# Performance work log

Hardware: AMD Instinct MI355X
Metric: run time of the kernel (lower is better)

The kernel has to match this reference:

```python
import jax, jax.numpy as jnp
import numpy as np

NUM_EXPERTS = 8
TOP_K = 2
B, S, D = 8, 8192, 256


def setup_inputs() -> dict:
    key = jax.random.key(0)
    ks = jax.random.split(key, 4)
    scale = 1.0 / np.sqrt(D).astype(np.float32)
    return {
        "input_embeddings": jax.random.normal(ks[0], (B, S, D), jnp.float32),
        "router_w": jax.random.normal(ks[1], (NUM_EXPERTS, D), jnp.float32) * scale,
        "w1": jax.random.normal(ks[2], (NUM_EXPERTS, D, D), jnp.float32) * scale,
        "b1": jnp.zeros((NUM_EXPERTS, D), jnp.float32),
        "w2": jax.random.normal(ks[3], (NUM_EXPERTS, D, D), jnp.float32) * scale,
        "b2": jnp.zeros((NUM_EXPERTS, D), jnp.float32),
    }


def _moe(tokens, router_w, w1, b1, w2, b2):
    # tokens: [N, D]
    N = tokens.shape[0]
    E = router_w.shape[0]
    # Router in float32 (matches torch .float() cast)
    logits = tokens.astype(jnp.float32) @ router_w.astype(jnp.float32).T  # [N, E]
    probs = jax.nn.softmax(logits, axis=-1)
    rw, re = jax.lax.top_k(probs, TOP_K)  # [N, K]
    if TOP_K > 1:
        rw = rw / jnp.maximum(rw.sum(-1, keepdims=True), 1e-12)
    rw = rw.astype(tokens.dtype)
    # Dense combine weights: zero for unselected experts -> identical math to
    # the torch gather/index_add dispatch (weight 0 == not routed).
    combine = jnp.zeros((N, E), tokens.dtype).at[jnp.arange(N)[:, None], re].set(rw)
    out = tokens  # residual: tokens + weighted expert outputs
    for e in range(E):  # small fixed expert loop
        h = jax.nn.gelu(tokens @ w1[e] + b1[e], approximate=False)
        y = h @ w2[e] + b2[e]
        out = out + combine[:, e:e + 1] * y
    return out


def reference(input_embeddings, router_w, w1, b1, w2, b2):
    b, s, d = input_embeddings.shape
    tokens = input_embeddings.reshape(b * s, d)
    return _moe(tokens, router_w, w1, b1, w2, b2).reshape(b, s, d)
```

## Files before the change

### kernel.cpp

```cpp
#include <hip/hip_runtime.h>
#include <hip/hip_bf16.h>

#define NEXP 8
#define DD 256

typedef __attribute__((ext_vector_type(8))) short  bf16x8;
typedef __attribute__((ext_vector_type(4))) float  f32x4;

__device__ __forceinline__ unsigned short f2bf(float f) {
    union { float f; unsigned int u; } v; v.f = f;
    unsigned int r = (v.u + 0x7FFFu + ((v.u >> 16) & 1u)) >> 16;
    return (unsigned short)r;
}

__device__ __forceinline__ float gelu_exact(float x) {
    return 0.5f * x * (1.0f + erff(x * 0.70710678118654752f));
}

__global__ __launch_bounds__(256)
void prep_weights(const float* __restrict__ w1, const float* __restrict__ w2,
                  unsigned short* __restrict__ w1t, unsigned short* __restrict__ w2t)
{
    __shared__ float tile[64][65];
    const int m  = blockIdx.x >> 7;
    const int e  = (blockIdx.x >> 4) & 7;
    const int ko = (blockIdx.x >> 2) & 3;
    const int no = blockIdx.x & 3;
    const float* src = m ? w2 : w1;
    unsigned short* dst = m ? w2t : w1t;
    const size_t base = ((size_t)e << 16);

    #pragma unroll
    for (int i = 0; i < 16; ++i) {
        int r = i * 4 + (threadIdx.x >> 6);
        int c = threadIdx.x & 63;
        tile[r][c] = src[base + (size_t)(ko * 64 + r) * DD + no * 64 + c];
    }
    __syncthreads();
    #pragma unroll
    for (int i = 0; i < 8; ++i) {
        int n  = i * 8 + (threadIdx.x >> 5);
        int k2 = (threadIdx.x & 31) * 2;
        unsigned int val = (unsigned int)f2bf(tile[k2][n])
                         | ((unsigned int)f2bf(tile[k2 + 1][n]) << 16);
        *(unsigned int*)(dst + base + (size_t)(no * 64 + n) * DD + ko * 64 + k2) = val;
    }
}

__global__ __launch_bounds__(256)
void router_kernel(const float* __restrict__ X, const float* __restrict__ RW,
                   unsigned int* __restrict__ re, float* __restrict__ rwgt,
                   int* __restrict__ bcnt, int N)
{
    __shared__ float rws[NEXP * DD];
    __shared__ int hist[16];
    const int tid = threadIdx.x;
    if (tid < 16) hist[tid] = 0;
    for (int i = tid; i < NEXP * DD / 4; i += 256)
        ((float4*)rws)[i] = ((const float4*)RW)[i];
    __syncthreads();
    const int wave = tid >> 6, lane = tid & 63;

    for (int it = 0; it < 16; ++it) {
        int t = blockIdx.x * 64 + wave * 16 + it;
        float4 xv = *(const float4*)(X + (size_t)t * DD + lane * 4);
        float lg[NEXP];
        #pragma unroll
        for (int e = 0; e < NEXP; ++e) {
            float4 wv = *(const float4*)(rws + e * DD + lane * 4);
            lg[e] = xv.x * wv.x + xv.y * wv.y + xv.z * wv.z + xv.w * wv.w;
        }
        #pragma unroll
        for (int e = 0; e < NEXP; ++e) {
            #pragma unroll
            for (int off = 32; off; off >>= 1)
                lg[e] += __shfl_xor(lg[e], off);
        }
        int e0 = 0; float l0 = lg[0];
        #pragma unroll
        for (int e = 1; e < NEXP; ++e) if (lg[e] > l0) { l0 = lg[e]; e0 = e; }
        int e1 = -1; float l1 = -3.4e38f;
        #pragma unroll
        for (int e = 0; e < NEXP; ++e) if (e != e0 && lg[e] > l1) { l1 = lg[e]; e1 = e; }
        float d   = expf(l1 - l0);
        float w0  = 1.0f / (1.0f + d);
        float w1v = d / (1.0f + d);
        if (lane == 0) {
            re[t] = (unsigned int)e0 | ((unsigned int)e1 << 8);
            rwgt[2 * t + 0] = w0;
            rwgt[2 * t + 1] = w1v;
            atomicAdd(&hist[e0], 1);
            atomicAdd(&hist[8 + e1], 1);
        }
    }
    __syncthreads();
    if (tid < 16) bcnt[blockIdx.x * 16 + tid] = hist[tid];
}

__global__ void scan_kernel(const int* __restrict__ bcnt, int* __restrict__ bbase,
                            int* __restrict__ cnt, int nchunk)
{
    int j = threadIdx.x;
    if (j >= 16) return;
    int run = 0;
    for (int c = 0; c < nchunk; ++c) {
        bbase[c * 16 + j] = run;
        run += bcnt[(4 * c + 0) * 16 + j] + bcnt[(4 * c + 1) * 16 + j]
             + bcnt[(4 * c + 2) * 16 + j] + bcnt[(4 * c + 3) * 16 + j];
    }
    cnt[j] = run;
}

__global__ __launch_bounds__(256)
void scatter_kernel(const unsigned int* __restrict__ re, const int* __restrict__ bbase,
                    unsigned int* __restrict__ lists, int N)
{
    __shared__ int hist[16];
    __shared__ int base[16];
    const int tid = threadIdx.x;
    if (tid < 16) { hist[tid] = 0; base[tid] = bbase[blockIdx.x * 16 + tid]; }
    __syncthreads();
    int t = blockIdx.x * 256 + tid;
    unsigned int r = re[t];
    int e0 = r & 255, e1 = (r >> 8) & 255;
    int r0 = atomicAdd(&hist[e0], 1);
    int r1 = atomicAdd(&hist[8 + e1], 1);
    lists[(size_t)e0 * N + base[e0] + r0] = (unsigned int)t;
    lists[(size_t)(8 + e1) * N + base[8 + e1] + r1] = (unsigned int)t;
}

template<int PASS>
__global__ __launch_bounds__(256, 3)
void expert_pass(const float* __restrict__ X, float* __restrict__ Out,
                 const unsigned short* __restrict__ W1t, const unsigned short* __restrict__ W2t,
                 const float* __restrict__ B1, const float* __restrict__ B2,
                 const unsigned int* __restrict__ lists, const float* __restrict__ rwgt,
                 const int* __restrict__ cnt, int N)
{
    const int e = blockIdx.y;
    const int count = cnt[PASS * NEXP + e];
    const int m0 = blockIdx.x * 64;
    if (m0 >= count) return;

    __shared__ unsigned char Ts[32768];

    const int tid = threadIdx.x;
    const unsigned int* listE = lists + (size_t)(PASS * NEXP + e) * N;

    #pragma unroll
    for (int i = 0; i < 16; ++i) {
        int id = i * 256 + tid;
        int row = id >> 6;
        int c4 = id & 63;
        int m = m0 + row;
        float4 v = make_float4(0.f, 0.f, 0.f, 0.f);
        if (m < count) {
            unsigned int t = listE[m];
            v = *(const float4*)(X + (size_t)t * DD + c4 * 4);
        }
        uint2 p;
        p.x = (unsigned int)f2bf(v.x) | ((unsigned int)f2bf(v.y) << 16);
        p.y = (unsigned int)f2bf(v.z) | ((unsigned int)f2bf(v.w) << 16);
        int byte = row * 512 + c4 * 8;
        byte ^= (row & 7) << 4;
        *(uint2*)(Ts + byte) = p;
    }
    __syncthreads();

    const int wv = tid >> 6;
    const int lane = tid & 63;
    const int c0 = wv * 64;
    const int lrow = lane & 15;
    const int lk = (lane >> 4) * 8;

    f32x4 acc[4][4] = {};
    const unsigned short* W1e = W1t + (size_t)e * DD * DD;
    for (int kk = 0; kk < 8; ++kk) {
        int kbase = kk * 32 + lk;
        bf16x8 a[4], b[4];
        #pragma unroll
        for (int rf = 0; rf < 4; ++rf) {
            int row = rf * 16 + lrow;
            int byte = (row * 512 + kbase * 2) ^ ((row & 7) << 4);
            a[rf] = *(const bf16x8*)(Ts + byte);
        }
        #pragma unroll
        for (int cf = 0; cf < 4; ++cf) {
            int col = c0 + cf * 16 + lrow;
            b[cf] = *(const bf16x8*)(W1e + (size_t)col * DD + kbase);
        }
        #pragma unroll
        for (int rf = 0; rf < 4; ++rf)
            #pragma unroll
            for (int cf = 0; cf < 4; ++cf)
                acc[rf][cf] = __builtin_amdgcn_mfma_f32_16x16x32_bf16(a[rf], b[cf], acc[rf][cf], 0, 0, 0);
    }
    __syncthreads();

    #pragma unroll
    for (int cf = 0; cf < 4; ++cf) {
        int col = c0 + cf * 16 + lrow;
        float bias = B1[e * DD + col];
        #pragma unroll
        for (int rf = 0; rf < 4; ++rf) {
            #pragma unroll
            for (int j = 0; j < 4; ++j) {
                int row = rf * 16 + (lane >> 4) * 4 + j;
                float h = gelu_exact(acc[rf][cf][j] + bias);
                int byte = (row * 512 + col * 2) ^ ((row & 7) << 4);
                *(unsigned short*)(Ts + byte) = f2bf(h);
            }
        }
    }
    __syncthreads();

    f32x4 acc2[4][4] = {};
    const unsigned short* W2e = W2t + (size_t)e * DD * DD;
    for (int kk = 0; kk < 8; ++kk) {
        int kbase = kk * 32 + lk;
        bf16x8 a[4], b[4];
        #pragma unroll
        for (int rf = 0; rf < 4; ++rf) {
            int row = rf * 16 + lrow;
            int byte = (row * 512 + kbase * 2) ^ ((row & 7) << 4);
            a[rf] = *(const bf16x8*)(Ts + byte);
        }
        #pragma unroll
        for (int cf = 0; cf < 4; ++cf) {
            int col = c0 + cf * 16 + lrow;
            b[cf] = *(const bf16x8*)(W2e + (size_t)col * DD + kbase);
        }
        #pragma unroll
        for (int rf = 0; rf < 4; ++rf)
            #pragma unroll
            for (int cf = 0; cf < 4; ++cf)
                acc2[rf][cf] = __builtin_amdgcn_mfma_f32_16x16x32_bf16(a[rf], b[cf], acc2[rf][cf], 0, 0, 0);
    }

    #pragma unroll
    for (int rf = 0; rf < 4; ++rf) {
        #pragma unroll
        for (int j = 0; j < 4; ++j) {
            int row = rf * 16 + (lane >> 4) * 4 + j;
            int m = m0 + row;
            if (m < count) {
                unsigned int t = listE[m];
                float wgt = rwgt[2 * t + PASS];
                #pragma unroll
                for (int cf = 0; cf < 4; ++cf) {
                    int col = c0 + cf * 16 + lrow;
                    float y = acc2[rf][cf][j] + B2[e * DD + col];
                    size_t idx = (size_t)t * DD + col;
                    if (PASS == 0) Out[idx] = X[idx] + wgt * y;
                    else           Out[idx] += wgt * y;
                }
            }
        }
    }
}

extern "C" void kernel_launch(void* const* d_in, const int* in_sizes, int n_in,
                              void* d_out, int out_size, void* d_ws, size_t ws_size,
                              hipStream_t stream) {
    const float* X  = (const float*)d_in[0];
    const float* RW = (const float*)d_in[1];
    const float* W1 = (const float*)d_in[2];
    const float* B1 = (const float*)d_in[3];
    const float* W2 = (const float*)d_in[4];
    const float* B2 = (const float*)d_in[5];
    float* Out = (float*)d_out;
    const int N = in_sizes[0] / DD;

    unsigned char* w = (unsigned char*)d_ws;
    size_t off = 0;
    int* cnt = (int*)(w + off);                   off += 256;
    unsigned int* re = (unsigned int*)(w + off);  off += (size_t)N * 4;
    float* rwgt = (float*)(w + off);              off += (size_t)N * 8;
    unsigned int* lists = (unsigned int*)(w + off); off += (size_t)2 * NEXP * N * 4;
    unsigned short* w1t = (unsigned short*)(w + off); off += (size_t)NEXP * DD * DD * 2;
    unsigned short* w2t = (unsigned short*)(w + off); off += (size_t)NEXP * DD * DD * 2;
    int* bcnt  = (int*)(w + off);                 off += (size_t)(N / 64) * 16 * 4;
    int* bbase = (int*)(w + off);                 off += (size_t)(N / 256) * 16 * 4;

    prep_weights<<<256, 256, 0, stream>>>(W1, W2, w1t, w2t);
    router_kernel<<<N / 64, 256, 0, stream>>>(X, RW, re, rwgt, bcnt, N);
    scan_kernel<<<1, 64, 0, stream>>>(bcnt, bbase, cnt, N / 256);
    scatter_kernel<<<N / 256, 256, 0, stream>>>(re, bbase, lists, N);
    dim3 grid((N + 63) / 64, NEXP);
    expert_pass<0><<<grid, 256, 0, stream>>>(X, Out, w1t, w2t, B1, B2, lists, rwgt, cnt, N);
    expert_pass<1><<<grid, 256, 0, stream>>>(X, Out, w1t, w2t, B1, B2, lists, rwgt, cnt, N);
}
```

Measured before the change: 416.0 us.

## Stage bf16 activations, merge expert passes into one grid, add combine kernel

The router now also writes a bf16 copy of the input tokens. A single expert kernel covers both top-k slots via a z-dimension and gathers the smaller bf16 rows instead of converting fp32 on the fly. Weighted expert outputs are written as bf16 per slot, and a separate elementwise kernel adds the residual and both slots. This removes the serialized second pass and halves gather bytes, at the cost of extra workspace traffic for the bf16 copies and an extra launch. It also rounds expert outputs to bf16 before the sum, which adds precision error. The path only runs when the workspace is large enough.

```diff
diff --git a/kernel.cpp b/kernel.cpp
--- a/kernel.cpp
+++ b/kernel.cpp
@@ -12,7 +12,9 @@
     unsigned int r = (v.u + 0x7FFFu + ((v.u >> 16) & 1u)) >> 16;
     return (unsigned short)r;
 }
-
+__device__ __forceinline__ float bf2f(unsigned int lo16) {
+    union { unsigned int u; float f; } v; v.u = lo16 << 16; return v.f;
+}
 __device__ __forceinline__ float gelu_exact(float x) {
     return 0.5f * x * (1.0f + erff(x * 0.70710678118654752f));
 }
@@ -50,7 +52,7 @@
 __global__ __launch_bounds__(256)
 void router_kernel(const float* __restrict__ X, const float* __restrict__ RW,
                    unsigned int* __restrict__ re, float* __restrict__ rwgt,
-                   int* __restrict__ bcnt, int N)
+                   int* __restrict__ bcnt, unsigned short* __restrict__ Xbf, int N)
 {
     __shared__ float rws[NEXP * DD];
     __shared__ int hist[16];
@@ -64,6 +66,12 @@
     for (int it = 0; it < 16; ++it) {
         int t = blockIdx.x * 64 + wave * 16 + it;
         float4 xv = *(const float4*)(X + (size_t)t * DD + lane * 4);
+        if (Xbf) {
+            uint2 p;
+            p.x = (unsigned int)f2bf(xv.x) | ((unsigned int)f2bf(xv.y) << 16);
+            p.y = (unsigned int)f2bf(xv.z) | ((unsigned int)f2bf(xv.w) << 16);
+            *(uint2*)(Xbf + (size_t)t * DD + lane * 4) = p;
+        }
         float lg[NEXP];
         #pragma unroll
         for (int e = 0; e < NEXP; ++e) {
@@ -129,6 +137,162 @@
     lists[(size_t)(8 + e1) * N + base[8 + e1] + r1] = (unsigned int)t;
 }
 
+__global__ __launch_bounds__(256, 5)
+void expert_y(const unsigned short* __restrict__ Xbf, unsigned short* __restrict__ Ybf,
+              const unsigned short* __restrict__ W1t, const unsigned short* __restrict__ W2t,
+              const float* __restrict__ B1, const float* __restrict__ B2,
+              const unsigned int* __restrict__ lists, const float* __restrict__ rwgt,
+              const int* __restrict__ cnt, int N)
+{
+    const int slot = blockIdx.z;
+    const int e = blockIdx.y;
+    const int count = cnt[slot * NEXP + e];
+    const int m0 = blockIdx.x * 64;
+    if (m0 >= count) return;
+
+    __shared__ unsigned char Ts[32768];
+
+    const int tid = threadIdx.x;
+    const unsigned int* listE = lists + (size_t)(slot * NEXP + e) * N;
+
+    {
+        unsigned int tok[16];
+        #pragma unroll
+        for (int i = 0; i < 16; ++i) {
+            int m = m0 + i * 4 + (tid >> 6);
+            tok[i] = (m < count) ? listE[m] : 0xFFFFFFFFu;
+        }
+        #pragma unroll
+        for (int i = 0; i < 16; ++i) {
+            int row = i * 4 + (tid >> 6);
+            uint2 v = make_uint2(0u, 0u);
+            if (tok[i] != 0xFFFFFFFFu)
+                v = *(const uint2*)(Xbf + (size_t)tok[i] * DD + (tid & 63) * 4);
+            int byte = (row * 512 + (tid & 63) * 8) ^ ((row & 7) << 4);
+            *(uint2*)(Ts + byte) = v;
+        }
+    }
+    __syncthreads();
+
+    const int wv = tid >> 6;
+    const int lane = tid & 63;
+    const int c0 = wv * 64;
+    const int lrow = lane & 15;
+    const int lk = (lane >> 4) * 8;
+
+    f32x4 acc[4][4] = {};
+    const unsigned short* W1e = W1t + (size_t)e * DD * DD;
+    for (int kk = 0; kk < 8; ++kk) {
+        int kbase = kk * 32 + lk;
+        bf16x8 a[4], b[4];
+        #pragma unroll
+        for (int rf = 0; rf < 4; ++rf) {
+            int row = rf * 16 + lrow;
+            int byte = (row * 512 + kbase * 2) ^ ((row & 7) << 4);
+            a[rf] = *(const bf16x8*)(Ts + byte);
+        }
+        #pragma unroll
+        for (int cf = 0; cf < 4; ++cf) {
+            int col = c0 + cf * 16 + lrow;
+            b[cf] = *(const bf16x8*)(W1e + (size_t)col * DD + kbase);
+        }
+        #pragma unroll
+        for (int rf = 0; rf < 4; ++rf)
+            #pragma unroll
+            for (int cf = 0; cf < 4; ++cf)
+                acc[rf][cf] = __builtin_amdgcn_mfma_f32_16x16x32_bf16(a[rf], b[cf], acc[rf][cf], 0, 0, 0);
+    }
+    __syncthreads();
+
+    #pragma unroll
+    for (int cf = 0; cf < 4; ++cf) {
+        int col = c0 + cf * 16 + lrow;
+        float bias = B1[e * DD + col];
+        #pragma unroll
+        for (int rf = 0; rf < 4; ++rf) {
+            #pragma unroll
+            for (int j = 0; j < 4; ++j) {
+                int row = rf * 16 + (lane >> 4) * 4 + j;
+                float h = gelu_exact(acc[rf][cf][j] + bias);
+                int byte = (row * 512 + col * 2) ^ ((row & 7) << 4);
+                *(unsigned short*)(Ts + byte) = f2bf(h);
+            }
+        }
+    }
+    __syncthreads();
+
+    f32x4 acc2[4][4] = {};
+    const unsigned short* W2e = W2t + (size_t)e * DD * DD;
+    for (int kk = 0; kk < 8; ++kk) {
+        int kbase = kk * 32 + lk;
+        bf16x8 a[4], b[4];
+        #pragma unroll
+        for (int rf = 0; rf < 4; ++rf) {
+            int row = rf * 16 + lrow;
+            int byte = (row * 512 + kbase * 2) ^ ((row & 7) << 4);
+            a[rf] = *(const bf16x8*)(Ts + byte);
+        }
+        #pragma unroll
+        for (int cf = 0; cf < 4; ++cf) {
+            int col = c0 + cf * 16 + lrow;
+            b[cf] = *(const bf16x8*)(W2e + (size_t)col * DD + kbase);
+        }
+        #pragma unroll
+        for (int rf = 0; rf < 4; ++rf)
+            #pragma unroll
+            for (int cf = 0; cf < 4; ++cf)
+                acc2[rf][cf] = __builtin_amdgcn_mfma_f32_16x16x32_bf16(a[rf], b[cf], acc2[rf][cf], 0, 0, 0);
+    }
+    __syncthreads();
+
+    #pragma unroll
+    for (int rf = 0; rf < 4; ++rf) {
+        #pragma unroll
+        for (int j = 0; j < 4; ++j) {
+            int row = rf * 16 + (lane >> 4) * 4 + j;
+            int m = m0 + row;
+            float wgt = 0.0f;
+            if (m < count) wgt = rwgt[2 * listE[m] + slot];
+            #pragma unroll
+            for (int cf = 0; cf < 4; ++cf) {
+                int col = c0 + cf * 16 + lrow;
+                float y = (acc2[rf][cf][j] + B2[e * DD + col]) * wgt;
+                int byte = (row * 512 + col * 2) ^ ((row & 7) << 4);
+                *(unsigned short*)(Ts + byte) = f2bf(y);
+            }
+        }
+    }
+    __syncthreads();
+
+    #pragma unroll
+    for (int i = 0; i < 16; ++i) {
+        int row = i * 4 + (tid >> 6);
+        int m = m0 + row;
+        if (m < count) {
+            unsigned int t = listE[m];
+            int byte = (row * 512 + (tid & 63) * 8) ^ ((row & 7) << 4);
+            uint2 v = *(const uint2*)(Ts + byte);
+            *(uint2*)(Ybf + ((size_t)slot * N + t) * DD + (tid & 63) * 4) = v;
+        }
+    }
+}
+
+__global__ __launch_bounds__(256)
+void combine_kernel(const float* __restrict__ X, const unsigned short* __restrict__ Ybf,
+                    float* __restrict__ Out, int N)
+{
+    size_t idx = (size_t)blockIdx.x * 256 + threadIdx.x;
+    float4 x = ((const float4*)X)[idx];
+    uint2 y0 = ((const uint2*)Ybf)[idx];
+    uint2 y1 = ((const uint2*)(Ybf + (size_t)N * DD))[idx];
+    float4 o;
+    o.x = x.x + bf2f(y0.x & 0xFFFFu) + bf2f(y1.x & 0xFFFFu);
+    o.y = x.y + bf2f(y0.x >> 16)     + bf2f(y1.x >> 16);
+    o.z = x.z + bf2f(y0.y & 0xFFFFu) + bf2f(y1.y & 0xFFFFu);
+    o.w = x.w + bf2f(y0.y >> 16)     + bf2f(y1.y >> 16);
+    ((float4*)Out)[idx] = o;
+}
+
 template<int PASS>
 __global__ __launch_bounds__(256, 3)
 void expert_pass(const float* __restrict__ X, float* __restrict__ Out,
@@ -161,8 +325,7 @@
         uint2 p;
         p.x = (unsigned int)f2bf(v.x) | ((unsigned int)f2bf(v.y) << 16);
         p.y = (unsigned int)f2bf(v.z) | ((unsigned int)f2bf(v.w) << 16);
-        int byte = row * 512 + c4 * 8;
-        byte ^= (row & 7) << 4;
+        int byte = (row * 512 + c4 * 8) ^ ((row & 7) << 4);
         *(uint2*)(Ts + byte) = p;
     }
     __syncthreads();
@@ -281,12 +444,24 @@
     unsigned short* w2t = (unsigned short*)(w + off); off += (size_t)NEXP * DD * DD * 2;
     int* bcnt  = (int*)(w + off);                 off += (size_t)(N / 64) * 16 * 4;
     int* bbase = (int*)(w + off);                 off += (size_t)(N / 256) * 16 * 4;
+    unsigned short* Xbf = (unsigned short*)(w + off); size_t off_xbf = off + (size_t)N * DD * 2;
+    unsigned short* Ybf = (unsigned short*)(w + off_xbf);
+    size_t off_total = off_xbf + (size_t)2 * N * DD * 2;
+
+    const bool big = (ws_size >= off_total);
 
     prep_weights<<<256, 256, 0, stream>>>(W1, W2, w1t, w2t);
-    router_kernel<<<N / 64, 256, 0, stream>>>(X, RW, re, rwgt, bcnt, N);
+    router_kernel<<<N / 64, 256, 0, stream>>>(X, RW, re, rwgt, bcnt, big ? Xbf : nullptr, N);
     scan_kernel<<<1, 64, 0, stream>>>(bcnt, bbase, cnt, N / 256);
     scatter_kernel<<<N / 256, 256, 0, stream>>>(re, bbase, lists, N);
-    dim3 grid((N + 63) / 64, NEXP);
-    expert_pass<0><<<grid, 256, 0, stream>>>(X, Out, w1t, w2t, B1, B2, lists, rwgt, cnt, N);
-    expert_pass<1><<<grid, 256, 0, stream>>>(X, Out, w1t, w2t, B1, B2, lists, rwgt, cnt, N);
-}
+
+    if (big) {
+        dim3 grid(N / 64, NEXP, 2);
+        expert_y<<<grid, 256, 0, stream>>>(Xbf, Ybf, w1t, w2t, B1, B2, lists, rwgt, cnt, N);
+        combine_kernel<<<N / 4, 256, 0, stream>>>(X, Ybf, Out, N);
+    } else {
+        dim3 grid(N / 64, NEXP);
+        expert_pass<0><<<grid, 256, 0, stream>>>(X, Out, w1t, w2t, B1, B2, lists, rwgt, cnt, N);
+        expert_pass<1><<<grid, 256, 0, stream>>>(X, Out, w1t, w2t, B1, B2, lists, rwgt, cnt, N);
+    }
+}
```

Result: slower. 711.3 us (+71.0%).
